# Performance work log

Hardware: AMD Instinct MI355X
Metric: run time of the kernel (lower is better)

Reference implementation:

```python
import jax, jax.numpy as jnp
import numpy as np

B, H, S, D = 8, 8, 1024, 64

def setup_inputs() -> dict:
    key = jax.random.key(0)
    kq, kk, kv = jax.random.split(key, 3)
    queries = jax.random.normal(kq, (B, H, S, D), dtype=jnp.float32)
    keys = jax.random.normal(kk, (B, H, S, D), dtype=jnp.float32)
    values = jax.random.normal(kv, (B, H, S, D), dtype=jnp.float32)
    return {"queries": queries, "keys": keys, "values": values}

def reference(queries, keys, values):
    # scale = 1/sqrt(D) since self.scale is None
    scale = 1.0 / jnp.sqrt(jnp.asarray(queries.shape[-1], queries.dtype))
    # scores: [B, H, S, S]
    scores = jnp.einsum("bhqd,bhkd->bhqk", queries, keys) * scale
    # mask_flag=False -> no masking; dropout treated as identity (eval mode)
    attn = jax.nn.softmax(scores, axis=-1)
    output = jnp.einsum("bhqk,bhkd->bhqd", attn, values)
    return (output, attn)
```

## Files before the change

### kernel.cpp

```cpp
#include <hip/hip_runtime.h>
#include <hip/hip_bf16.h>

#define B_ 8
#define H_ 8
#define S_ 1024
#define D_ 64

typedef __attribute__((ext_vector_type(8))) short bf16x8;
typedef __attribute__((ext_vector_type(4))) short bf16x4;
typedef __attribute__((ext_vector_type(4))) float f32x4;

__device__ __forceinline__ short f2bf(float f) {
  union { float f; unsigned u; } x; x.f = f;
  unsigned r = (x.u + 0x7FFFu + ((x.u >> 16) & 1u)) >> 16;
  return (short)r;
}

__global__ __launch_bounds__(256) void cvt_qk(const float* __restrict__ Q,
                                              const float* __restrict__ K,
                                              short* __restrict__ Qb,
                                              short* __restrict__ Kb) {
  const float* in = blockIdx.y ? K : Q;
  short* out      = blockIdx.y ? Kb : Qb;
  const size_t i = ((size_t)blockIdx.x * 256 + threadIdx.x) * 8;
  float4 a = *(const float4*)(in + i);
  float4 b = *(const float4*)(in + i + 4);
  bf16x8 f;
  f[0] = f2bf(a.x); f[1] = f2bf(a.y); f[2] = f2bf(a.z); f[3] = f2bf(a.w);
  f[4] = f2bf(b.x); f[5] = f2bf(b.y); f[6] = f2bf(b.z); f[7] = f2bf(b.w);
  *(bf16x8*)(out + i) = f;
}

__global__ __launch_bounds__(256) void vtrans(const float* __restrict__ V,
                                              short* __restrict__ Vt) {
  const int bh = blockIdx.y;
  const int s0 = blockIdx.x * 64;
  __shared__ float tile[64][65];
  const float* Vb = V + ((size_t)bh * S_ + s0) * D_;
  const int t = threadIdx.x;
  {
    const int rbase = t >> 4;
    const int c4 = (t & 15) * 4;
    #pragma unroll
    for (int i = 0; i < 4; ++i) {
      const int row = i * 16 + rbase;
      float4 v = *(const float4*)(Vb + (size_t)row * D_ + c4);
      tile[row][c4 + 0] = v.x; tile[row][c4 + 1] = v.y;
      tile[row][c4 + 2] = v.z; tile[row][c4 + 3] = v.w;
    }
  }
  __syncthreads();
  const int d = t >> 2;
  const int sq = (t & 3) * 16;
  short* op = Vt + ((size_t)bh * D_ + d) * S_ + s0 + sq;
  bf16x8 a, b;
  #pragma unroll
  for (int j = 0; j < 8; ++j) {
    a[j] = f2bf(tile[sq + j][d]);
    b[j] = f2bf(tile[sq + 8 + j][d]);
  }
  *(bf16x8*)op = a;
  *(bf16x8*)(op + 8) = b;
}

constexpr int QT  = 16;
constexpr int NW  = 4;
constexpr int TPW = (S_ / 16) / NW;

__global__ __launch_bounds__(256, 4) void attn_fused(
    const short* __restrict__ Qb16, const short* __restrict__ Kb16,
    const short* __restrict__ Vt,
    float* __restrict__ O, float* __restrict__ A)
{
  const int nwg = (S_ / QT) * B_ * H_;
  const int cpx = nwg / 8;
  const int lin = blockIdx.x;
  const int swz = (lin & 7) * cpx + (lin >> 3);
  const int bh  = swz / (S_ / QT);
  const int q0  = (swz % (S_ / QT)) * QT;

  const int tid  = threadIdx.x;
  const int wave = tid >> 6;
  const int lane = tid & 63;
  const int m    = lane & 15;
  const int quad = lane >> 4;

  const short* Qb  = Qb16 + (size_t)bh * S_ * D_;
  const short* Kb  = Kb16 + (size_t)bh * S_ * D_;
  const short* Vtb = Vt   + (size_t)bh * D_ * S_;
  float* Ob = O + (size_t)bh * S_ * D_;
  float* Ab = A + (size_t)bh * S_ * S_;

  __shared__ float redmax[NW][QT];
  __shared__ float redsum[NW][QT];
  __shared__ float obuf[NW][QT][D_ + 4];

  bf16x8 qf0, qf1;
  {
    const short* qp = Qb + (size_t)(q0 + m) * D_ + quad * 8;
    qf0 = *(const bf16x8*)qp;
    qf1 = *(const bf16x8*)(qp + 32);
  }

  f32x4 acc[TPW];
  #pragma unroll
  for (int t = 0; t < TPW; ++t) {
    const int kt = t * NW + wave;
    const short* kp = Kb + (size_t)(kt * 16 + m) * D_ + quad * 8;
    bf16x8 kf0 = *(const bf16x8*)kp;
    bf16x8 kf1 = *(const bf16x8*)(kp + 32);
    f32x4 c = {0.f, 0.f, 0.f, 0.f};
    c = __builtin_amdgcn_mfma_f32_16x16x32_bf16(kf0, qf0, c, 0, 0, 0);
    c = __builtin_amdgcn_mfma_f32_16x16x32_bf16(kf1, qf1, c, 0, 0, 0);
    acc[t] = c;
  }

  float vmax = acc[0][0];
  #pragma unroll
  for (int t = 0; t < TPW; ++t) {
    #pragma unroll
    for (int r = 0; r < 4; ++r) vmax = fmaxf(vmax, acc[t][r]);
  }
  vmax = fmaxf(vmax, __shfl_xor(vmax, 16));
  vmax = fmaxf(vmax, __shfl_xor(vmax, 32));
  if (lane < 16) redmax[wave][lane] = vmax;
  __syncthreads();
  const float gm = fmaxf(fmaxf(redmax[0][m], redmax[1][m]),
                         fmaxf(redmax[2][m], redmax[3][m]));

  constexpr float CE = 0.125f * 1.4426950408889634f;
  float s = 0.f;
  #pragma unroll
  for (int t = 0; t < TPW; ++t) {
    #pragma unroll
    for (int r = 0; r < 4; ++r) {
      float e = __builtin_exp2f((acc[t][r] - gm) * CE);
      acc[t][r] = e;
      s += e;
    }
  }
  s += __shfl_xor(s, 16);
  s += __shfl_xor(s, 32);
  if (lane < 16) redsum[wave][lane] = s;
  __syncthreads();
  const float rinv = 1.f / ((redsum[0][m] + redsum[1][m]) +
                            (redsum[2][m] + redsum[3][m]));

  f32x4 oc0 = {0.f,0.f,0.f,0.f}, oc1 = {0.f,0.f,0.f,0.f};
  f32x4 oc2 = {0.f,0.f,0.f,0.f}, oc3 = {0.f,0.f,0.f,0.f};
  #pragma unroll
  for (int t = 0; t < TPW; ++t) {
    const int kt = t * NW + wave;
    f32x4 pn = acc[t] * rinv;
    __builtin_nontemporal_store(pn,
        (f32x4*)&Ab[(size_t)(q0 + m) * S_ + kt * 16 + quad * 4]);
    bf16x4 pa;
    pa[0] = f2bf(pn[0]); pa[1] = f2bf(pn[1]);
    pa[2] = f2bf(pn[2]); pa[3] = f2bf(pn[3]);
    const short* vp = Vtb + (size_t)m * S_ + kt * 16 + quad * 4;
    bf16x4 bv0 = *(const bf16x4*)(vp);
    bf16x4 bv1 = *(const bf16x4*)(vp + (size_t)16 * S_);
    bf16x4 bv2 = *(const bf16x4*)(vp + (size_t)32 * S_);
    bf16x4 bv3 = *(const bf16x4*)(vp + (size_t)48 * S_);
    oc0 = __builtin_amdgcn_mfma_f32_16x16x16bf16_1k(pa, bv0, oc0, 0, 0, 0);
    oc1 = __builtin_amdgcn_mfma_f32_16x16x16bf16_1k(pa, bv1, oc1, 0, 0, 0);
    oc2 = __builtin_amdgcn_mfma_f32_16x16x16bf16_1k(pa, bv2, oc2, 0, 0, 0);
    oc3 = __builtin_amdgcn_mfma_f32_16x16x16bf16_1k(pa, bv3, oc3, 0, 0, 0);
  }

  #pragma unroll
  for (int r = 0; r < 4; ++r) {
    obuf[wave][quad * 4 + r][m]      = oc0[r];
    obuf[wave][quad * 4 + r][16 + m] = oc1[r];
    obuf[wave][quad * 4 + r][32 + m] = oc2[r];
    obuf[wave][quad * 4 + r][48 + m] = oc3[r];
  }
  __syncthreads();
  {
    const int q  = tid >> 4;
    const int d4 = (tid & 15) * 4;
    f32x4 o0 = *(const f32x4*)&obuf[0][q][d4];
    f32x4 o1 = *(const f32x4*)&obuf[1][q][d4];
    f32x4 o2 = *(const f32x4*)&obuf[2][q][d4];
    f32x4 o3 = *(const f32x4*)&obuf[3][q][d4];
    f32x4 o = (o0 + o1) + (o2 + o3);
    *(f32x4*)&Ob[(size_t)(q0 + q) * D_ + d4] = o;
  }
}

extern "C" void kernel_launch(void* const* d_in, const int* in_sizes, int n_in,
                              void* d_out, int out_size, void* d_ws, size_t ws_size,
                              hipStream_t stream) {
  const float* Q = (const float*)d_in[0];
  const float* K = (const float*)d_in[1];
  const float* V = (const float*)d_in[2];
  float* O = (float*)d_out;
  float* A = O + (size_t)B_ * H_ * S_ * D_;

  const size_t NEL = (size_t)B_ * H_ * S_ * D_;
  short* Qbf = (short*)d_ws;
  short* Kbf = Qbf + NEL;
  short* Vtb = Kbf + NEL;

  const int cvt_blocks = (int)(NEL / 8 / 256);
  cvt_qk<<<dim3(cvt_blocks, 2), 256, 0, stream>>>(Q, K, Qbf, Kbf);
  vtrans<<<dim3(S_ / 64, B_ * H_), 256, 0, stream>>>(V, Vtb);

  attn_fused<<<(S_ / QT) * B_ * H_, NW * 64, 0, stream>>>(Qbf, Kbf, Vtb, O, A);
}
```

Baseline: 462.4 us.

## Software-prefetch K/V tiles and merge softmax reductions into one barrier

Loads the K and V fragments three tiles ahead in rotating register buffers so global-load latency overlaps the MFMA work. The softmax now computes per-wave local max and sum together and rescales them after a single block barrier, online-softmax style, replacing two barriers. Max and sum reductions become tree-shaped to shorten dependency chains. The prefetch buffers raise register pressure, which may reduce occupancy under the 4-blocks launch bound.

```diff
diff --git a/kernel.cpp b/kernel.cpp
--- a/kernel.cpp
+++ b/kernel.cpp
@@ -102,70 +102,106 @@
     qf1 = *(const bf16x8*)(qp + 32);
   }
 
+  const short* kbase = Kb + (size_t)m * D_ + quad * 8;
   f32x4 acc[TPW];
+  bf16x8 ka0[4], ka1[4];
+  #pragma unroll
+  for (int p = 0; p < 3; ++p) {
+    const short* kp = kbase + (size_t)((p * NW + wave) * 16) * D_;
+    ka0[p] = *(const bf16x8*)kp;
+    ka1[p] = *(const bf16x8*)(kp + 32);
+  }
   #pragma unroll
   for (int t = 0; t < TPW; ++t) {
-    const int kt = t * NW + wave;
-    const short* kp = Kb + (size_t)(kt * 16 + m) * D_ + quad * 8;
-    bf16x8 kf0 = *(const bf16x8*)kp;
-    bf16x8 kf1 = *(const bf16x8*)(kp + 32);
+    if (t + 3 < TPW) {
+      const short* kp = kbase + (size_t)(((t + 3) * NW + wave) * 16) * D_;
+      ka0[(t + 3) & 3] = *(const bf16x8*)kp;
+      ka1[(t + 3) & 3] = *(const bf16x8*)(kp + 32);
+    }
     f32x4 c = {0.f, 0.f, 0.f, 0.f};
-    c = __builtin_amdgcn_mfma_f32_16x16x32_bf16(kf0, qf0, c, 0, 0, 0);
-    c = __builtin_amdgcn_mfma_f32_16x16x32_bf16(kf1, qf1, c, 0, 0, 0);
+    c = __builtin_amdgcn_mfma_f32_16x16x32_bf16(ka0[t & 3], qf0, c, 0, 0, 0);
+    c = __builtin_amdgcn_mfma_f32_16x16x32_bf16(ka1[t & 3], qf1, c, 0, 0, 0);
     acc[t] = c;
   }
 
-  float vmax = acc[0][0];
-  #pragma unroll
-  for (int t = 0; t < TPW; ++t) {
-    #pragma unroll
-    for (int r = 0; r < 4; ++r) vmax = fmaxf(vmax, acc[t][r]);
-  }
+  float mx[TPW];
+  #pragma unroll
+  for (int t = 0; t < TPW; ++t)
+    mx[t] = fmaxf(fmaxf(acc[t][0], acc[t][1]), fmaxf(acc[t][2], acc[t][3]));
+  #pragma unroll
+  for (int sstep = TPW / 2; sstep > 0; sstep >>= 1) {
+    #pragma unroll
+    for (int t = 0; t < sstep; ++t) mx[t] = fmaxf(mx[t], mx[t + sstep]);
+  }
+  float vmax = mx[0];
   vmax = fmaxf(vmax, __shfl_xor(vmax, 16));
   vmax = fmaxf(vmax, __shfl_xor(vmax, 32));
-  if (lane < 16) redmax[wave][lane] = vmax;
+
+  constexpr float CE = 0.125f * 1.4426950408889634f;
+  float sm[TPW];
+  #pragma unroll
+  for (int t = 0; t < TPW; ++t) {
+    float e0 = __builtin_exp2f((acc[t][0] - vmax) * CE);
+    float e1 = __builtin_exp2f((acc[t][1] - vmax) * CE);
+    float e2 = __builtin_exp2f((acc[t][2] - vmax) * CE);
+    float e3 = __builtin_exp2f((acc[t][3] - vmax) * CE);
+    acc[t][0] = e0; acc[t][1] = e1; acc[t][2] = e2; acc[t][3] = e3;
+    sm[t] = (e0 + e1) + (e2 + e3);
+  }
+  #pragma unroll
+  for (int sstep = TPW / 2; sstep > 0; sstep >>= 1) {
+    #pragma unroll
+    for (int t = 0; t < sstep; ++t) sm[t] += sm[t + sstep];
+  }
+  float psum = sm[0];
+  psum += __shfl_xor(psum, 16);
+  psum += __shfl_xor(psum, 32);
+
+  if (lane < 16) {
+    redmax[wave][lane] = vmax;
+    redsum[wave][lane] = psum;
+  }
   __syncthreads();
-  const float gm = fmaxf(fmaxf(redmax[0][m], redmax[1][m]),
-                         fmaxf(redmax[2][m], redmax[3][m]));
-
-  constexpr float CE = 0.125f * 1.4426950408889634f;
-  float s = 0.f;
-  #pragma unroll
-  for (int t = 0; t < TPW; ++t) {
-    #pragma unroll
-    for (int r = 0; r < 4; ++r) {
-      float e = __builtin_exp2f((acc[t][r] - gm) * CE);
-      acc[t][r] = e;
-      s += e;
-    }
-  }
-  s += __shfl_xor(s, 16);
-  s += __shfl_xor(s, 32);
-  if (lane < 16) redsum[wave][lane] = s;
-  __syncthreads();
-  const float rinv = 1.f / ((redsum[0][m] + redsum[1][m]) +
-                            (redsum[2][m] + redsum[3][m]));
+
+  float m0 = redmax[0][m], m1 = redmax[1][m], m2 = redmax[2][m], m3 = redmax[3][m];
+  const float gmax = fmaxf(fmaxf(m0, m1), fmaxf(m2, m3));
+  float sumg = redsum[0][m] * __builtin_exp2f((m0 - gmax) * CE)
+             + redsum[1][m] * __builtin_exp2f((m1 - gmax) * CE)
+             + redsum[2][m] * __builtin_exp2f((m2 - gmax) * CE)
+             + redsum[3][m] * __builtin_exp2f((m3 - gmax) * CE);
+  const float rinv = __builtin_exp2f((vmax - gmax) * CE) / sumg;
+
+  const short* vbase = Vtb + (size_t)m * S_ + quad * 4;
+  bf16x4 vb[4][4];
+  #pragma unroll
+  for (int p = 0; p < 3; ++p) {
+    const short* vp = vbase + (p * NW + wave) * 16;
+    #pragma unroll
+    for (int i = 0; i < 4; ++i)
+      vb[p][i] = *(const bf16x4*)(vp + (size_t)(16 * i) * S_);
+  }
 
   f32x4 oc0 = {0.f,0.f,0.f,0.f}, oc1 = {0.f,0.f,0.f,0.f};
   f32x4 oc2 = {0.f,0.f,0.f,0.f}, oc3 = {0.f,0.f,0.f,0.f};
+  float* arow = Ab + (size_t)(q0 + m) * S_ + quad * 4;
   #pragma unroll
   for (int t = 0; t < TPW; ++t) {
+    if (t + 3 < TPW) {
+      const short* vp = vbase + ((t + 3) * NW + wave) * 16;
+      #pragma unroll
+      for (int i = 0; i < 4; ++i)
+        vb[(t + 3) & 3][i] = *(const bf16x4*)(vp + (size_t)(16 * i) * S_);
+    }
     const int kt = t * NW + wave;
     f32x4 pn = acc[t] * rinv;
-    __builtin_nontemporal_store(pn,
-        (f32x4*)&Ab[(size_t)(q0 + m) * S_ + kt * 16 + quad * 4]);
+    __builtin_nontemporal_store(pn, (f32x4*)(arow + kt * 16));
     bf16x4 pa;
     pa[0] = f2bf(pn[0]); pa[1] = f2bf(pn[1]);
     pa[2] = f2bf(pn[2]); pa[3] = f2bf(pn[3]);
-    const short* vp = Vtb + (size_t)m * S_ + kt * 16 + quad * 4;
-    bf16x4 bv0 = *(const bf16x4*)(vp);
-    bf16x4 bv1 = *(const bf16x4*)(vp + (size_t)16 * S_);
-    bf16x4 bv2 = *(const bf16x4*)(vp + (size_t)32 * S_);
-    bf16x4 bv3 = *(const bf16x4*)(vp + (size_t)48 * S_);
-    oc0 = __builtin_amdgcn_mfma_f32_16x16x16bf16_1k(pa, bv0, oc0, 0, 0, 0);
-    oc1 = __builtin_amdgcn_mfma_f32_16x16x16bf16_1k(pa, bv1, oc1, 0, 0, 0);
-    oc2 = __builtin_amdgcn_mfma_f32_16x16x16bf16_1k(pa, bv2, oc2, 0, 0, 0);
-    oc3 = __builtin_amdgcn_mfma_f32_16x16x16bf16_1k(pa, bv3, oc3, 0, 0, 0);
+    oc0 = __builtin_amdgcn_mfma_f32_16x16x16bf16_1k(pa, vb[t & 3][0], oc0, 0, 0, 0);
+    oc1 = __builtin_amdgcn_mfma_f32_16x16x16bf16_1k(pa, vb[t & 3][1], oc1, 0, 0, 0);
+    oc2 = __builtin_amdgcn_mfma_f32_16x16x16bf16_1k(pa, vb[t & 3][2], oc2, 0, 0, 0);
+    oc3 = __builtin_amdgcn_mfma_f32_16x16x16bf16_1k(pa, vb[t & 3][3], oc3, 0, 0, 0);
   }
 
   #pragma unroll
```

Result: no change. 471.5 us (+2.0%).
